# Optimization experiments

Measured on AMD Instinct MI355X. Metric: run time of the kernel, lower is better.

## Reference

```python
import jax, jax.numpy as jnp
import numpy as np

D_MODEL = 1024
NUM_HEADS = 16
D_K = D_MODEL // NUM_HEADS
THETA = 10000.0
B, S = 2, 2048


def apply_rope(x, token_position, theta=THETA):
    # x: [B, H, S, d_k]; token_position: [B, S] int
    d_k = x.shape[-1]
    inv_freq = 1.0 / theta ** (jnp.arange(0, d_k, 2, dtype=jnp.float32) / d_k)  # [d_k/2]
    angles = token_position.astype(jnp.float32)[:, :, None] * inv_freq[None, None, :]  # [B,S,d_k/2]
    cos = jnp.cos(angles)[:, None, :, :]  # [B,1,S,d_k/2]
    sin = jnp.sin(angles)[:, None, :, :]
    x_even = x[..., 0::2]
    x_odd = x[..., 1::2]
    rot_even = x_even * cos - x_odd * sin
    rot_odd = x_even * sin + x_odd * cos
    # interleave back: stack on new last axis, then flatten
    return jnp.stack([rot_even, rot_odd], axis=-1).reshape(x.shape)


def setup_inputs() -> dict:
    key = jax.random.key(0)
    kx, kq, kk, kv, ko = jax.random.split(key, 5)
    scale = 1.0 / np.sqrt(D_MODEL)
    x = jax.random.normal(kx, (B, S, D_MODEL), dtype=jnp.float32)
    WQ = jax.random.normal(kq, (D_MODEL, D_MODEL), dtype=jnp.float32) * scale
    WK = jax.random.normal(kk, (D_MODEL, D_MODEL), dtype=jnp.float32) * scale
    WV = jax.random.normal(kv, (D_MODEL, D_MODEL), dtype=jnp.float32) * scale
    WO = jax.random.normal(ko, (D_MODEL, D_MODEL), dtype=jnp.float32) * scale
    token_position = jnp.broadcast_to(jnp.arange(S, dtype=jnp.int32)[None, :], (B, S))
    return {"x": x, "token_position": token_position, "WQ": WQ, "WK": WK, "WV": WV, "WO": WO}


def reference(x, token_position, WQ, WK, WV, WO):
    Batch, seq, _ = x.shape
    Q = jnp.einsum('bsd,de->bse', x, WQ).reshape(Batch, seq, NUM_HEADS, D_K).transpose(0, 2, 1, 3)
    K = jnp.einsum('bsd,de->bse', x, WK).reshape(Batch, seq, NUM_HEADS, D_K).transpose(0, 2, 1, 3)
    V = jnp.einsum('bsd,de->bse', x, WV).reshape(Batch, seq, NUM_HEADS, D_K).transpose(0, 2, 1, 3)
    Q = apply_rope(Q, token_position)
    K = apply_rope(K, token_position)
    score = jnp.einsum('bhqd,bhkd->bhqk', Q, K) / jnp.sqrt(jnp.float32(D_K))
    causal = jnp.tril(jnp.ones((seq, seq), dtype=bool))  # [S,S]
    score = jnp.where(causal[None, None, :, :], score, -jnp.inf)
    probs = jax.nn.softmax(score, axis=-1)
    out = jnp.einsum('bhqk,bhkd->bhqd', probs, V)
    out = out.transpose(0, 2, 1, 3).reshape(Batch, seq, D_MODEL)
    return jnp.einsum('bsd,de->bse', out, WO)
```

## Files before the change

kernel.cpp:

```cpp
#include <hip/hip_runtime.h>
#include <hip/hip_bf16.h>

typedef __attribute__((ext_vector_type(8))) short short8;
typedef __attribute__((ext_vector_type(4))) float f32x4;
typedef __hip_bfloat16 bf16_t;

#define SEQ 2048
#define DM 1024
#define NH 16
#define DK 64
#define NKT 16

static __device__ __forceinline__ f32x4 mfma16x16x32(short8 a, short8 b, f32x4 c) {
  return __builtin_amdgcn_mfma_f32_16x16x32_bf16(a, b, c, 0, 0, 0);
}

typedef const __attribute__((address_space(1))) unsigned int ga_u32_t;
typedef __attribute__((address_space(3))) unsigned int lds_u32_t;
static __device__ __forceinline__ void gld16(const bf16_t* g, bf16_t* l) {
  __builtin_amdgcn_global_load_lds((ga_u32_t*)g, (lds_u32_t*)l, 16, 0, 0);
}
static __device__ __forceinline__ void bar() { asm volatile("s_barrier" ::: "memory"); }
static __device__ __forceinline__ void wait_vm8() { asm volatile("s_waitcnt vmcnt(8)" ::: "memory"); }
static __device__ __forceinline__ void wait_vm0() { asm volatile("s_waitcnt vmcnt(0)" ::: "memory"); }

static __device__ __forceinline__ void stage_tile(const bf16_t* asrc, const bf16_t* bsrc,
                                                  char* bufbase, int w, int kk) {
#pragma unroll
  for (int j = 0; j < 4; ++j) {
    gld16(asrc + (size_t)(j * 32) * DM + kk, (bf16_t*)(bufbase + j * 4096 + w * 1024));
    gld16(bsrc + (size_t)(j * 32) * DM + kk, (bf16_t*)(bufbase + 16384 + j * 4096 + w * 1024));
  }
}

__global__ void sniff_dtype(const unsigned int* __restrict__ x, int* __restrict__ flag) {
  int lane = threadIdx.x & 63;
  int cnt = 0;
  for (int r = 0; r < 4; ++r) {
    unsigned int v = x[lane + r * 64];
    int e = (v >> 7) & 0xFF;
    if (e >= 100 && e <= 145) cnt++;
  }
  for (int d = 1; d < 64; d <<= 1) cnt += __shfl_xor(cnt, d, 64);
  if (lane == 0) *flag = (cnt >= 192) ? 1 : 0;
}

__global__ __launch_bounds__(256) void prep(const void* __restrict__ x,
                                            bf16_t* __restrict__ Xc,
                                            const void* __restrict__ w0,
                                            const void* __restrict__ w1,
                                            const void* __restrict__ w2,
                                            const void* __restrict__ w3,
                                            bf16_t* __restrict__ wt_base,
                                            const int* __restrict__ tokpos,
                                            float2* __restrict__ rtab,
                                            const int* __restrict__ flag) {
  int f = *flag;
  int bx = blockIdx.x, t = threadIdx.x;
  __shared__ bf16_t tile[64][65];
  if (bx < 4096) {
    int i = bx * 256 + t;
    if (f) {
      ((uint2*)Xc)[i] = ((const uint2*)x)[i];
    } else {
      const float4 v = ((const float4*)x)[i];
      bf16_t o[4] = {__float2bfloat16(v.x), __float2bfloat16(v.y),
                     __float2bfloat16(v.z), __float2bfloat16(v.w)};
      ((uint2*)Xc)[i] = *(const uint2*)o;
    }
  } else if (bx < 5120) {
    int rem = bx - 4096;
    int z = rem >> 8, bxx = rem & 15, byy = (rem >> 4) & 15;
    const void* src = (z == 0) ? w0 : (z == 1) ? w1 : (z == 2) ? w2 : w3;
    bf16_t* dst = wt_base + (size_t)((z + 1) & 3) * DM * DM;
    int tx = t & 63, ty = t >> 6;
    int r0 = byy * 64, c0 = bxx * 64;
    for (int i = 0; i < 64; i += 4) {
      size_t idx = (size_t)(r0 + ty + i) * DM + c0 + tx;
      tile[ty + i][tx] = f ? ((const bf16_t*)src)[idx]
                           : __float2bfloat16(((const float*)src)[idx]);
    }
    __syncthreads();
    for (int i = 0; i < 64; i += 4)
      dst[(size_t)(c0 + ty + i) * DM + r0 + tx] = tile[tx][ty + i];
  } else {
    int i = (bx - 5120) * 256 + t;
    int m = i >> 5, pp = i & 31;
    float pos = (float)tokpos[m];
    float invf = __powf(10000.0f, -(float)pp * (1.0f / 32.0f));
    float sn, cs;
    sincosf(pos * invf, &sn, &cs);
    rtab[i] = make_float2(cs, sn);
  }
}

__global__ __launch_bounds__(256) void gemm128_qkv(const bf16_t* __restrict__ A,
                                                   const bf16_t* __restrict__ WTqkv,
                                                   bf16_t* __restrict__ Qb,
                                                   bf16_t* __restrict__ Kb,
                                                   bf16_t* __restrict__ VTo,
                                                   const float2* __restrict__ rtab) {
  extern __shared__ char smem[];
  int t = threadIdx.x;
  int w = t >> 6, lane = t & 63, l15 = lane & 15, quad = lane >> 4;
  int wrow = w >> 1, wcol = w & 1;
  int m0 = blockIdx.y * 128, nx = blockIdx.x, n0 = nx * 128;
  int srow0 = w * 8 + (lane >> 3);
  int scg = (lane & 7) ^ (lane >> 3);
  const bf16_t* asrc = A + (size_t)(m0 + srow0) * DM + scg * 8;
  const bf16_t* bsrc = WTqkv + (size_t)(n0 + srow0) * DM + scg * 8;

  f32x4 acc[4][4] = {};
  stage_tile(asrc, bsrc, smem, w, 0);
  stage_tile(asrc, bsrc, smem + 32768, w, 64);
  for (int kt = 0; kt < NKT; ++kt) {
    if (kt < NKT - 1) wait_vm8(); else wait_vm0();
    bar();
    if (kt + 2 < NKT)
      stage_tile(asrc, bsrc, smem + ((kt + 2) % 3) * 32768, w, (kt + 2) * 64);
    const bf16_t* Ab = (const bf16_t*)(smem + (kt % 3) * 32768);
    const bf16_t* Bb = Ab + 8192;
    short8 af[4][2], bfr[4][2];
#pragma unroll
    for (int mt = 0; mt < 4; ++mt) {
      int r = wrow * 64 + mt * 16 + l15;
      af[mt][0] = *(const short8*)(Ab + r * 64 + ((quad ^ (l15 & 7)) * 8));
      af[mt][1] = *(const short8*)(Ab + r * 64 + (((4 + quad) ^ (l15 & 7)) * 8));
    }
#pragma unroll
    for (int nt = 0; nt < 4; ++nt) {
      int r = wcol * 64 + nt * 16 + l15;
      bfr[nt][0] = *(const short8*)(Bb + r * 64 + ((quad ^ (l15 & 7)) * 8));
      bfr[nt][1] = *(const short8*)(Bb + r * 64 + (((4 + quad) ^ (l15 & 7)) * 8));
    }
#pragma unroll
    for (int mt = 0; mt < 4; ++mt)
#pragma unroll
      for (int nt = 0; nt < 4; ++nt) {
        acc[mt][nt] = mfma16x16x32(af[mt][0], bfr[nt][0], acc[mt][nt]);
        acc[mt][nt] = mfma16x16x32(af[mt][1], bfr[nt][1], acc[mt][nt]);
      }
  }

  int sel = nx >> 3;
  int nc = (nx & 7) * 128;
  __syncthreads();
  bf16_t (*Tw)[72] = (bf16_t(*)[72])(smem + w * 9216);
  int b = m0 >> 11;
  int h = (nc >> 6) + wcol;
  if (sel < 2) {
    bf16_t* dst = sel ? Kb : Qb;
    float sgnv = (l15 & 1) ? 1.0f : -1.0f;
#pragma unroll
    for (int mt = 0; mt < 4; ++mt)
#pragma unroll
      for (int r = 0; r < 4; ++r) {
        int m = m0 + wrow * 64 + mt * 16 + quad * 4 + r;
        const float2* tr = rtab + m * 32;
#pragma unroll
        for (int nt = 0; nt < 4; ++nt) {
          int d = nt * 16 + l15;
          float val = acc[mt][nt][r];
          float partner = __shfl_xor(val, 1, 64);
          float2 cssn = tr[d >> 1];
          Tw[mt * 16 + quad * 4 + r][d] = __float2bfloat16(val * cssn.x + sgnv * partner * cssn.y);
        }
      }
    int s_base = (m0 & (SEQ - 1)) + wrow * 64;
    bf16_t* dq = dst + ((size_t)(b * NH + h) * SEQ + s_base) * DK;
#pragma unroll
    for (int c = 0; c < 8; ++c) {
      int row = c * 8 + (lane >> 3);
      int col = (lane & 7) * 8;
      *(short8*)&dq[(size_t)row * DK + col] = *(const short8*)&Tw[row][col];
    }
  } else {
#pragma unroll
    for (int mt = 0; mt < 4; ++mt)
#pragma unroll
      for (int nt = 0; nt < 4; ++nt)
#pragma unroll
        for (int r = 0; r < 4; ++r)
          Tw[nt * 16 + l15][mt * 16 + quad * 4 + r] = __float2bfloat16(acc[mt][nt][r]);
    int s_base = m0 & (SEQ - 1);
#pragma unroll
    for (int c = 0; c < 4; ++c) {
      int d = c * 16 + (lane >> 2);
      int s2 = (lane & 3) * 16;
      size_t ob = ((size_t)(b * NH + h) * DK + d) * SEQ + s_base + wrow * 64 + s2;
      *(short8*)&VTo[ob] = *(const short8*)&Tw[d][s2];
      *(short8*)&VTo[ob + 8] = *(const short8*)&Tw[d][s2 + 8];
    }
  }
}

__global__ __launch_bounds__(256) void gemm128_out(const bf16_t* __restrict__ A,
                                                   const bf16_t* __restrict__ BT,
                                                   void* __restrict__ out,
                                                   const int* __restrict__ flag) {
  extern __shared__ char smem[];
  int f = *flag;
  int t = threadIdx.x;
  int w = t >> 6, lane = t & 63, l15 = lane & 15, quad = lane >> 4;
  int wrow = w >> 1, wcol = w & 1;
  int m0 = blockIdx.y * 128, n0 = blockIdx.x * 128;
  int srow0 = w * 8 + (lane >> 3);
  int scg = (lane & 7) ^ (lane >> 3);
  const bf16_t* asrc = A + (size_t)(m0 + srow0) * DM + scg * 8;
  const bf16_t* bsrc = BT + (size_t)(n0 + srow0) * DM + scg * 8;

  f32x4 acc[4][4] = {};
  stage_tile(asrc, bsrc, smem, w, 0);
  stage_tile(asrc, bsrc, smem + 32768, w, 64);
  for (int kt = 0; kt < NKT; ++kt) {
    if (kt < NKT - 1) wait_vm8(); else wait_vm0();
    bar();
    if (kt + 2 < NKT)
      stage_tile(asrc, bsrc, smem + ((kt + 2) % 3) * 32768, w, (kt + 2) * 64);
    const bf16_t* Ab = (const bf16_t*)(smem + (kt % 3) * 32768);
    const bf16_t* Bb = Ab + 8192;
    short8 af[4][2], bfr[4][2];
#pragma unroll
    for (int mt = 0; mt < 4; ++mt) {
      int r = wrow * 64 + mt * 16 + l15;
      af[mt][0] = *(const short8*)(Ab + r * 64 + ((quad ^ (l15 & 7)) * 8));
      af[mt][1] = *(const short8*)(Ab + r * 64 + (((4 + quad) ^ (l15 & 7)) * 8));
    }
#pragma unroll
    for (int nt = 0; nt < 4; ++nt) {
      int r = wcol * 64 + nt * 16 + l15;
      bfr[nt][0] = *(const short8*)(Bb + r * 64 + ((quad ^ (l15 & 7)) * 8));
      bfr[nt][1] = *(const short8*)(Bb + r * 64 + (((4 + quad) ^ (l15 & 7)) * 8));
    }
#pragma unroll
    for (int mt = 0; mt < 4; ++mt)
#pragma unroll
      for (int nt = 0; nt < 4; ++nt) {
        acc[mt][nt] = mfma16x16x32(af[mt][0], bfr[nt][0], acc[mt][nt]);
        acc[mt][nt] = mfma16x16x32(af[mt][1], bfr[nt][1], acc[mt][nt]);
      }
  }
#pragma unroll
  for (int mt = 0; mt < 4; ++mt)
#pragma unroll
    for (int nt = 0; nt < 4; ++nt)
#pragma unroll
      for (int r = 0; r < 4; ++r) {
        int m = m0 + wrow * 64 + mt * 16 + quad * 4 + r;
        int col = n0 + wcol * 64 + nt * 16 + l15;
        size_t oidx = (size_t)m * DM + col;
        if (f) ((bf16_t*)out)[oidx] = __float2bfloat16(acc[mt][nt][r]);
        else   ((float*)out)[oidx] = acc[mt][nt][r];
      }
}

__global__ __launch_bounds__(256) void attn_fwd(const bf16_t* __restrict__ Q,
                                                const bf16_t* __restrict__ K,
                                                const bf16_t* __restrict__ VT,
                                                bf16_t* __restrict__ O) {
  int x = blockIdx.x, bh = blockIdx.y;
  int b = bh >> 4, h = bh & 15;
  int g = x + (bh << 4);
  int raw = (g + (g >> 8)) & 15;
  const int pmap[16] = {0, 15, 1, 13, 2, 12, 3, 11, 4, 10, 5, 9, 6, 8, 7, 14};
  int p = pmap[raw];
  int qA = p, qB = 31 - p;
  int t = threadIdx.x;
  int w = t >> 6, lane = t & 63, l15 = lane & 15, quad = lane >> 4;
  const size_t base = (size_t)bh * SEQ * DK;
  const bf16_t* Qp = Q + base;
  const bf16_t* Kp = K + base;
  const bf16_t* VTp = VT + base;

  __shared__ __align__(16) bf16_t Ks[64][72];
  __shared__ __align__(16) bf16_t Vs[64][72];
  __shared__ __align__(16) bf16_t Pb[4][2][16][72];

  int rowA = qA * 64 + w * 16 + l15;
  int rowB = qB * 64 + w * 16 + l15;
  short8 qfA0 = *(const short8*)(Qp + (size_t)rowA * DK + quad * 8);
  short8 qfA1 = *(const short8*)(Qp + (size_t)rowA * DK + 32 + quad * 8);
  short8 qfB0 = *(const short8*)(Qp + (size_t)rowB * DK + quad * 8);
  short8 qfB1 = *(const short8*)(Qp + (size_t)rowB * DK + 32 + quad * 8);

  int srow = t >> 2, scoff = (t & 3) * 16;
  const bf16_t* kst = Kp + (size_t)srow * DK + scoff;
  const bf16_t* vst = VTp + (size_t)srow * SEQ + scoff;

  short8 kA = *(const short8*)(kst);
  short8 kB = *(const short8*)(kst + 8);
  short8 vA = *(const short8*)(vst);
  short8 vB = *(const short8*)(vst + 8);

  f32x4 oA[4] = {}, oB[4] = {};
  float rA[4] = {0.f, 0.f, 0.f, 0.f}, rB[4] = {0.f, 0.f, 0.f, 0.f};

  for (int kb = 0; kb <= qB; ++kb) {
    __syncthreads();
    *(short8*)&Ks[srow][scoff] = kA;
    *(short8*)&Ks[srow][scoff + 8] = kB;
    *(short8*)&Vs[srow][scoff] = vA;
    *(short8*)&Vs[srow][scoff + 8] = vB;
    __syncthreads();

    int nkb = (kb < qB) ? (kb + 1) : qB;
    kA = *(const short8*)(kst + (size_t)nkb * 64 * DK);
    kB = *(const short8*)(kst + (size_t)nkb * 64 * DK + 8);
    vA = *(const short8*)(vst + (size_t)nkb * 64);
    vB = *(const short8*)(vst + (size_t)nkb * 64 + 8);

    bool doA = (kb <= qA);

    {
      f32x4 sc[4];
#pragma unroll
      for (int kt = 0; kt < 4; ++kt) {
        f32x4 a = {};
        a = mfma16x16x32(qfB0, *(const short8*)&Ks[kt * 16 + l15][quad * 8], a);
        a = mfma16x16x32(qfB1, *(const short8*)&Ks[kt * 16 + l15][32 + quad * 8], a);
        sc[kt] = a;
      }
      bool diag = (kb == qB);
#pragma unroll
      for (int kt = 0; kt < 4; ++kt)
#pragma unroll
        for (int reg = 0; reg < 4; ++reg) {
          float sv = sc[kt][reg] * 0.125f;
          if (diag) {
            int kg = kt * 16 + l15, qg = w * 16 + quad * 4 + reg;
            if (kg > qg) sv = -30000.0f;
          }
          float pp = __expf(sv);
          rB[reg] += pp;
          Pb[w][1][quad * 4 + reg][kt * 16 + l15] = __float2bfloat16(pp);
        }
      short8 p0 = *(const short8*)&Pb[w][1][l15][quad * 8];
      short8 p1 = *(const short8*)&Pb[w][1][l15][32 + quad * 8];
#pragma unroll
      for (int dt = 0; dt < 4; ++dt) {
        oB[dt] = mfma16x16x32(p0, *(const short8*)&Vs[dt * 16 + l15][quad * 8], oB[dt]);
        oB[dt] = mfma16x16x32(p1, *(const short8*)&Vs[dt * 16 + l15][32 + quad * 8], oB[dt]);
      }
    }
    if (doA) {
      f32x4 sc[4];
#pragma unroll
      for (int kt = 0; kt < 4; ++kt) {
        f32x4 a = {};
        a = mfma16x16x32(qfA0, *(const short8*)&Ks[kt * 16 + l15][quad * 8], a);
        a = mfma16x16x32(qfA1, *(const short8*)&Ks[kt * 16 + l15][32 + quad * 8], a);
        sc[kt] = a;
      }
      bool diag = (kb == qA);
#pragma unroll
      for (int kt = 0; kt < 4; ++kt)
#pragma unroll
        for (int reg = 0; reg < 4; ++reg) {
          float sv = sc[kt][reg] * 0.125f;
          if (diag) {
            int kg = kt * 16 + l15, qg = w * 16 + quad * 4 + reg;
            if (kg > qg) sv = -30000.0f;
          }
          float pp = __expf(sv);
          rA[reg] += pp;
          Pb[w][0][quad * 4 + reg][kt * 16 + l15] = __float2bfloat16(pp);
        }
      short8 p0 = *(const short8*)&Pb[w][0][l15][quad * 8];
      short8 p1 = *(const short8*)&Pb[w][0][l15][32 + quad * 8];
#pragma unroll
      for (int dt = 0; dt < 4; ++dt) {
        oA[dt] = mfma16x16x32(p0, *(const short8*)&Vs[dt * 16 + l15][quad * 8], oA[dt]);
        oA[dt] = mfma16x16x32(p1, *(const short8*)&Vs[dt * 16 + l15][32 + quad * 8], oA[dt]);
      }
    }
  }

  for (int d = 1; d < 16; d <<= 1)
#pragma unroll
    for (int reg = 0; reg < 4; ++reg) {
      rA[reg] += __shfl_xor(rA[reg], d, 64);
      rB[reg] += __shfl_xor(rB[reg], d, 64);
    }

#pragma unroll
  for (int dt = 0; dt < 4; ++dt)
#pragma unroll
    for (int reg = 0; reg < 4; ++reg) {
      int col = h * DK + dt * 16 + l15;
      int qa = qA * 64 + w * 16 + quad * 4 + reg;
      int qb_ = qB * 64 + w * 16 + quad * 4 + reg;
      O[((size_t)b * SEQ + qa) * DM + col] = __float2bfloat16(oA[dt][reg] / rA[reg]);
      O[((size_t)b * SEQ + qb_) * DM + col] = __float2bfloat16(oB[dt][reg] / rB[reg]);
    }
}

extern "C" void kernel_launch(void* const* d_in, const int* in_sizes, int n_in,
                              void* d_out, int out_size, void* d_ws, size_t ws_size,
                              hipStream_t stream) {
  const void* x = d_in[0];
  const int* tokpos = (const int*)d_in[1];
  const void* WQ = d_in[2];
  const void* WK = d_in[3];
  const void* WV = d_in[4];
  const void* WO = d_in[5];

  char* ws = (char*)d_ws;
  const size_t MB = 1024 * 1024;
  bf16_t* WT  = (bf16_t*)ws;
  bf16_t* Xc  = (bf16_t*)(ws + 8 * MB);
  bf16_t* Qb  = (bf16_t*)(ws + 16 * MB);
  bf16_t* Kb  = (bf16_t*)(ws + 24 * MB);
  bf16_t* VTb = (bf16_t*)(ws + 32 * MB);
  bf16_t* Ab  = (bf16_t*)(ws + 8 * MB);
  int* flag   = (int*)(ws + 40 * MB);
  float2* rtab = (float2*)(ws + 41 * MB);

  dim3 blk(256);
  const size_t gemm_lds = 3 * 32768;
  sniff_dtype<<<1, 64, 0, stream>>>((const unsigned int*)x, flag);
  prep<<<5632, blk, 0, stream>>>(x, Xc, WQ, WK, WV, WO, WT, tokpos, rtab, flag);
  gemm128_qkv<<<dim3(24, 32), blk, gemm_lds, stream>>>(Xc, WT + (size_t)DM * DM, Qb, Kb, VTb, rtab);
  attn_fwd<<<dim3(16, 32), blk, 0, stream>>>(Qb, Kb, VTb, Ab);
  gemm128_out<<<dim3(8, 32), blk, gemm_lds, stream>>>(Ab, WT, d_out, flag);
}
```

Before: 196.5 us.

## Replace triple-buffered async GEMM staging with single static LDS buffer

Both GEMM kernels drop the three-stage global-to-LDS prefetch ring, which used manual vmcnt waits and raw barriers, in favour of one statically sized LDS tile. Each k-step now loads that tile and synchronises before and after it. This cuts per-block LDS from 96 KB to about 32–36 KB, which could allow more resident blocks per CU. In exchange, global-load latency is no longer overlapped with MFMA work, and each k-step pays two full barriers.

```diff
diff --git a/kernel.cpp b/kernel.cpp
--- a/kernel.cpp
+++ b/kernel.cpp
@@ -20,9 +20,6 @@
 static __device__ __forceinline__ void gld16(const bf16_t* g, bf16_t* l) {
   __builtin_amdgcn_global_load_lds((ga_u32_t*)g, (lds_u32_t*)l, 16, 0, 0);
 }
-static __device__ __forceinline__ void bar() { asm volatile("s_barrier" ::: "memory"); }
-static __device__ __forceinline__ void wait_vm8() { asm volatile("s_waitcnt vmcnt(8)" ::: "memory"); }
-static __device__ __forceinline__ void wait_vm0() { asm volatile("s_waitcnt vmcnt(0)" ::: "memory"); }
 
 static __device__ __forceinline__ void stage_tile(const bf16_t* asrc, const bf16_t* bsrc,
                                                   char* bufbase, int w, int kk) {
@@ -100,7 +97,7 @@
                                                    bf16_t* __restrict__ Kb,
                                                    bf16_t* __restrict__ VTo,
                                                    const float2* __restrict__ rtab) {
-  extern __shared__ char smem[];
+  __shared__ __align__(16) char smem[36864];
   int t = threadIdx.x;
   int w = t >> 6, lane = t & 63, l15 = lane & 15, quad = lane >> 4;
   int wrow = w >> 1, wcol = w & 1;
@@ -111,14 +108,11 @@
   const bf16_t* bsrc = WTqkv + (size_t)(n0 + srow0) * DM + scg * 8;
 
   f32x4 acc[4][4] = {};
-  stage_tile(asrc, bsrc, smem, w, 0);
-  stage_tile(asrc, bsrc, smem + 32768, w, 64);
   for (int kt = 0; kt < NKT; ++kt) {
-    if (kt < NKT - 1) wait_vm8(); else wait_vm0();
-    bar();
-    if (kt + 2 < NKT)
-      stage_tile(asrc, bsrc, smem + ((kt + 2) % 3) * 32768, w, (kt + 2) * 64);
-    const bf16_t* Ab = (const bf16_t*)(smem + (kt % 3) * 32768);
+    __syncthreads();
+    stage_tile(asrc, bsrc, smem, w, kt * 64);
+    __syncthreads();
+    const bf16_t* Ab = (const bf16_t*)smem;
     const bf16_t* Bb = Ab + 8192;
     short8 af[4][2], bfr[4][2];
 #pragma unroll
@@ -198,7 +192,7 @@
                                                    const bf16_t* __restrict__ BT,
                                                    void* __restrict__ out,
                                                    const int* __restrict__ flag) {
-  extern __shared__ char smem[];
+  __shared__ __align__(16) char smem[32768];
   int f = *flag;
   int t = threadIdx.x;
   int w = t >> 6, lane = t & 63, l15 = lane & 15, quad = lane >> 4;
@@ -210,14 +204,11 @@
   const bf16_t* bsrc = BT + (size_t)(n0 + srow0) * DM + scg * 8;
 
   f32x4 acc[4][4] = {};
-  stage_tile(asrc, bsrc, smem, w, 0);
-  stage_tile(asrc, bsrc, smem + 32768, w, 64);
   for (int kt = 0; kt < NKT; ++kt) {
-    if (kt < NKT - 1) wait_vm8(); else wait_vm0();
-    bar();
-    if (kt + 2 < NKT)
-      stage_tile(asrc, bsrc, smem + ((kt + 2) % 3) * 32768, w, (kt + 2) * 64);
-    const bf16_t* Ab = (const bf16_t*)(smem + (kt % 3) * 32768);
+    __syncthreads();
+    stage_tile(asrc, bsrc, smem, w, kt * 64);
+    __syncthreads();
+    const bf16_t* Ab = (const bf16_t*)smem;
     const bf16_t* Bb = Ab + 8192;
     short8 af[4][2], bfr[4][2];
 #pragma unroll
@@ -416,10 +407,9 @@
   float2* rtab = (float2*)(ws + 41 * MB);
 
   dim3 blk(256);
-  const size_t gemm_lds = 3 * 32768;
   sniff_dtype<<<1, 64, 0, stream>>>((const unsigned int*)x, flag);
   prep<<<5632, blk, 0, stream>>>(x, Xc, WQ, WK, WV, WO, WT, tokpos, rtab, flag);
-  gemm128_qkv<<<dim3(24, 32), blk, gemm_lds, stream>>>(Xc, WT + (size_t)DM * DM, Qb, Kb, VTb, rtab);
+  gemm128_qkv<<<dim3(24, 32), blk, 0, stream>>>(Xc, WT + (size_t)DM * DM, Qb, Kb, VTb, rtab);
   attn_fwd<<<dim3(16, 32), blk, 0, stream>>>(Qb, Kb, VTb, Ab);
-  gemm128_out<<<dim3(8, 32), blk, gemm_lds, stream>>>(Ab, WT, d_out, flag);
-}
+  gemm128_out<<<dim3(8, 32), blk, 0, stream>>>(Ab, WT, d_out, flag);
+}
```

After: 200.9 us. +2.3%, slower.
